# Kernel optimization log

Hardware: AMD Instinct MI355X
Metric: run time of the kernel (lower is better)

Reference implementation:

```python
import jax, jax.numpy as jnp
import numpy as np

E = 4      # num_ensemble
DIN = 256  # input_dim
D = 256    # d_model (output_dim)
B = 16
T = 1024
LN_EPS = 1e-5


def setup_inputs() -> dict:
    key = jax.random.key(0)
    ks = jax.random.split(key, 14)
    s = 0.02
    x = jax.random.normal(ks[0], (B, T, DIN), dtype=jnp.float32)
    in_proj_w = s * jax.random.normal(ks[1], (3, E, DIN, D), dtype=jnp.float32)
    in_proj_b = jnp.zeros((3, E, D), dtype=jnp.float32)
    mid_w = s * jax.random.normal(ks[2], (2, E, D, D), dtype=jnp.float32)
    mid_b = jnp.zeros((2, E, D), dtype=jnp.float32)
    ff_w1 = s * jax.random.normal(ks[3], (E, D, D), dtype=jnp.float32)
    ff_b1 = jnp.zeros((E, D), dtype=jnp.float32)
    ff_w2 = s * jax.random.normal(ks[4], (E, D, D), dtype=jnp.float32)
    ff_b2 = jnp.zeros((E, D), dtype=jnp.float32)
    ln_w = jnp.ones((E, D), dtype=jnp.float32)
    ln_b = jnp.zeros((E, D), dtype=jnp.float32)
    # LRU initializer (r_min=0.9, r_max=0.999)
    r_min, r_max = 0.9, 0.999
    u1 = jax.random.uniform(ks[5], (E, D), dtype=jnp.float32)
    u2 = jax.random.uniform(ks[6], (E, D), dtype=jnp.float32)
    nu_log = jnp.log(-0.5 * jnp.log(u1 * (r_max ** 2 - r_min ** 2) + r_min ** 2))
    theta_log = jnp.log(u2 * 2.0 * np.pi)
    # |lambda|^2 = exp(-2*exp(nu_log))
    gamma_log = jnp.log(jnp.sqrt(1.0 - jnp.exp(-2.0 * jnp.exp(nu_log))))
    params_log = jnp.stack([nu_log, theta_log, gamma_log], axis=0)  # (3,E,D)
    return {"x": x, "in_proj_w": in_proj_w, "in_proj_b": in_proj_b,
            "params_log": params_log, "mid_w": mid_w, "mid_b": mid_b,
            "ff_w1": ff_w1, "ff_b1": ff_b1, "ff_w2": ff_w2, "ff_b2": ff_b2,
            "ln_w": ln_w, "ln_b": ln_b}


def _forward(x, in_proj_w, in_proj_b, params_log, mid_w, mid_b,
             ff_w1, ff_b1, ff_w2, ff_b2, ln_w, ln_b):
    # in_proj: 3 ensemble linears -> u: (3, E, B, T, D)
    u = jnp.einsum('bti,keio->kebto', x, in_proj_w) + in_proj_b[:, :, None, None, :]
    input_real, input_imag, o = u[0], u[1], u[2]

    params = jnp.exp(params_log)           # (3,E,D)
    nu, theta, gamma = params[0], params[1], params[2]
    mag = jnp.exp(-nu)
    f_real = mag * jnp.cos(theta)          # (E,D)
    f_imag = mag * jnp.sin(theta)

    ir = gamma[:, None, None, :] * input_real  # (E,B,T,D)
    ii = gamma[:, None, None, :] * input_imag

    # complex linear recurrence h_t = f * h_{t-1} + u_t over time axis
    fr = f_real[:, None, :]                # (E,1,D) broadcast over B
    fi = f_imag[:, None, :]
    ir_t = jnp.moveaxis(ir, 2, 0)          # (T,E,B,D)
    ii_t = jnp.moveaxis(ii, 2, 0)

    def step(carry, ut):
        hr, hi = carry
        ur, ui = ut
        hr2 = fr * hr - fi * hi + ur
        hi2 = fr * hi + fi * hr + ui
        return (hr2, hi2), (hr2, hi2)

    h0 = (jnp.zeros((E, B, D), x.dtype), jnp.zeros((E, B, D), x.dtype))
    (hr_last, hi_last), (out_r_t, out_i_t) = jax.lax.scan(step, h0, (ir_t, ii_t))
    output_real = jnp.moveaxis(out_r_t, 0, 2)  # (E,B,T,D)
    output_imag = jnp.moveaxis(out_i_t, 0, 2)

    # hidden packing: (1, B, 2*E*D) with ensemble blocks concatenated, real then imag
    hr_pack = jnp.transpose(hr_last, (1, 0, 2)).reshape(B, E * D)
    hi_pack = jnp.transpose(hi_last, (1, 0, 2)).reshape(B, E * D)
    hidden = jnp.concatenate([hr_pack, hi_pack], axis=-1)[None]  # (1,B,2ED)

    # middle_proj: 2 ensemble linears applied to (real, imag)
    stacked = jnp.stack([output_real, output_imag], axis=0)  # (2,E,B,T,D)
    mid = jnp.einsum('kebtd,kedo->kebto', stacked, mid_w) + mid_b[:, :, None, None, :]
    out = mid[0] - mid[1] + o                                # (E,B,T,D)

    # EnsemblePositionWiseFeedForward (dropout=0 -> identity)
    h1 = jax.nn.gelu(jnp.einsum('ebtd,edo->ebto', out, ff_w1)
                     + ff_b1[:, None, None, :], approximate=False)
    h2 = jnp.einsum('ebtd,edo->ebto', h1, ff_w2) + ff_b2[:, None, None, :] + out
    # LayerNorm over joint (E, D) dims for each (b, t)
    mean = jnp.mean(h2, axis=(0, 3), keepdims=True)
    var = jnp.var(h2, axis=(0, 3), keepdims=True)
    out_ln = (h2 - mean) / jnp.sqrt(var + LN_EPS)
    out_ln = out_ln * ln_w[:, None, None, :] + ln_b[:, None, None, :]
    return out_ln, hidden


def reference(x, in_proj_w, in_proj_b, params_log, mid_w, mid_b,
              ff_w1, ff_b1, ff_w2, ff_b2, ln_w, ln_b):
    return _forward(x, in_proj_w, in_proj_b, params_log, mid_w, mid_b,
                    ff_w1, ff_b1, ff_w2, ff_b2, ln_w, ln_b)
```

## Files before the change

### kernel.cpp

```cpp
#include <hip/hip_runtime.h>
#include <stdint.h>

#define BT_ 16384
#define TT  1024
#define CHUNKS 32
#define CLEN   32
#define LANES  16384

typedef __bf16 bf16x8 __attribute__((ext_vector_type(8)));
typedef float  f32x4  __attribute__((ext_vector_type(4)));
typedef unsigned int u32x4 __attribute__((ext_vector_type(4)));
typedef unsigned short u16;

__device__ __forceinline__ float b2f(u16 s){
    union { float f; unsigned int u; } c; c.u = ((unsigned int)s) << 16; return c.f;
}
__device__ __forceinline__ u16 f2b(float f){
    union { float f; unsigned int u; } c; c.f = f;
    unsigned int u = c.u;
    return (u16)((u + 0x7fffu + ((u >> 16) & 1u)) >> 16);
}

__device__ __forceinline__ void gload_lds16(const u16* g, u16* lds){
    __builtin_amdgcn_global_load_lds(
        (const __attribute__((address_space(1))) void*)g,
        (__attribute__((address_space(3))) void*)lds, 16, 0, 0);
}

__global__ __launch_bounds__(256) void conv_k(const float* __restrict__ x, u16* __restrict__ xc)
{
    long i = ((long)blockIdx.x * 256 + threadIdx.x) * 8;
    float4 v0 = *reinterpret_cast<const float4*>(x + i);
    float4 v1 = *reinterpret_cast<const float4*>(x + i + 4);
    union { u16 s[8]; u32x4 v; } p;
    p.s[0] = f2b(v0.x); p.s[1] = f2b(v0.y); p.s[2] = f2b(v0.z); p.s[3] = f2b(v0.w);
    p.s[4] = f2b(v1.x); p.s[5] = f2b(v1.y); p.s[6] = f2b(v1.z); p.s[7] = f2b(v1.w);
    *reinterpret_cast<u32x4*>(xc + i) = p.v;
}

__global__ __launch_bounds__(256) void prep_w(
    const float* __restrict__ ipw, const float* __restrict__ mw,
    const float* __restrict__ fw1, const float* __restrict__ fw2,
    u16* __restrict__ d_ipw, u16* __restrict__ d_mw,
    u16* __restrict__ d_fw1, u16* __restrict__ d_fw2)
{
    __shared__ u16 tile[64][72];
    int blk = blockIdx.x;
    int w = blk >> 4, t = blk & 15;
    int tr = (t >> 2) * 64;
    int tc = (t & 3) * 64;
    const float* src; u16* dst; int ostride; float sign = 1.f;
    if (w < 12)      { src = ipw + (size_t)w * 65536; dst = d_ipw + (size_t)w * 65536; ostride = 256; }
    else if (w < 20) { int u = w - 12, c = u >> 2, e = u & 3;
                       src = mw + (size_t)u * 65536;
                       dst = d_mw + (size_t)e * 131072 + c * 256; ostride = 512;
                       if (c) sign = -1.f; }
    else if (w < 24) { int e = w - 20; src = fw1 + (size_t)e * 65536; dst = d_fw1 + (size_t)e * 65536; ostride = 256; }
    else             { int e = w - 24; src = fw2 + (size_t)e * 65536; dst = d_fw2 + (size_t)e * 65536; ostride = 256; }

    int q = threadIdx.x;
    int r = q >> 2, cb = (q & 3) * 16;
#pragma unroll
    for (int j = 0; j < 4; j++) {
        int col = cb + j * 4;
        const float4 v = *reinterpret_cast<const float4*>(src + (size_t)(tr + r) * 256 + tc + col);
        tile[r][col + 0] = f2b(v.x * sign);
        tile[r][col + 1] = f2b(v.y * sign);
        tile[r][col + 2] = f2b(v.z * sign);
        tile[r][col + 3] = f2b(v.w * sign);
    }
    __syncthreads();
    int ol = q >> 2, ib = (q & 3) * 16;
    union { u16 s[8]; u32x4 v; } p0, p1;
#pragma unroll
    for (int k = 0; k < 8; k++) { p0.s[k] = tile[ib + k][ol]; p1.s[k] = tile[ib + 8 + k][ol]; }
    u16* drow = dst + (size_t)(tc + ol) * ostride + tr + ib;
    *reinterpret_cast<u32x4*>(drow)     = p0.v;
    *reinterpret_cast<u32x4*>(drow + 8) = p1.v;
}

__global__ __launch_bounds__(256, 3) void gemm_k(
    const u16* __restrict__ A0, const u16* __restrict__ B0,
    const float* __restrict__ biasf, const u16* __restrict__ aux,
    const float* __restrict__ gamlogf, u16* __restrict__ out0,
    u16* __restrict__ out1, int K, int mode, int MT)
{
    __shared__ __align__(16) u16 Bs[64 * 256];
    __shared__ __align__(16) float fs_all[4][1024];

    int tid  = threadIdx.x;
    int wave = tid >> 6, lane = tid & 63;
    int quad = lane >> 4, l16 = lane & 15;
    int n0 = blockIdx.y * 64;
    int z = blockIdx.z;
    int e, k3 = 0;
    const u16* A;
    const u16* Bm;
    if (mode == 1) { k3 = z >> 2; e = z & 3; A = A0; }
    else           { e = z; A = A0 + (size_t)e * BT_ * K; }
    Bm = B0 + (size_t)(mode == 1 ? z : e) * 256 * K;

    int srow = lane >> 5, schunk = lane & 31;
    int nhalf = K >> 8;

    float bias_nf[4], gam_nf[4];
#pragma unroll
    for (int nf = 0; nf < 4; nf++) {
        int col = n0 + nf * 16 + l16;
        if (mode == 1) {
            bias_nf[nf] = biasf[z * 256 + col];
            gam_nf[nf] = (k3 < 2) ? expf(gamlogf[2048 + e * 256 + col]) : 1.f;
        } else if (mode == 2) {
            bias_nf[nf] = biasf[e * 256 + col] - biasf[1024 + e * 256 + col];
        } else {
            bias_nf[nf] = biasf[e * 256 + col];
        }
    }

    float* fs = fs_all[wave];
    int rr = lane >> 3, ch = lane & 7;

    for (int mt = 0; mt < MT; mt++) {
        int m0 = (blockIdx.x * MT + mt) * 128;

        f32x4 acc[2][4];
#pragma unroll
        for (int i = 0; i < 2; i++)
#pragma unroll
            for (int j = 0; j < 4; j++) acc[i][j] = (f32x4){0.f, 0.f, 0.f, 0.f};

        for (int kh = 0; kh < nhalf; kh++) {
            if (nhalf > 1 || mt == 0) {
                if (mt || kh) __syncthreads();
#pragma unroll
                for (int i = 0; i < 8; i++) {
                    int row = wave * 16 + i * 2 + srow;
                    int c = schunk ^ (row & 7);
                    gload_lds16(Bm + (size_t)(n0 + row) * K + kh * 256 + c * 8,
                                &Bs[(wave * 16 + i * 2) * 256]);
                }
                __syncthreads();
            }

            const u16* Arow0 = A + (size_t)(m0 + wave * 32 + l16) * K + kh * 256 + quad * 8;
            const u16* Arow1 = Arow0 + (size_t)16 * K;

            bf16x8 a0[8], a1[8];
#pragma unroll
            for (int p = 0; p < 4; p++) {
                union { u32x4 v; bf16x8 b; } u0, u1;
                u0.v = *reinterpret_cast<const u32x4*>(Arow0 + p * 32); a0[p] = u0.b;
                u1.v = *reinterpret_cast<const u32x4*>(Arow1 + p * 32); a1[p] = u1.b;
            }
#pragma unroll
            for (int kt = 0; kt < 8; kt++) {
                if (kt < 4) {
                    union { u32x4 v; bf16x8 b; } u0, u1;
                    u0.v = *reinterpret_cast<const u32x4*>(Arow0 + (kt + 4) * 32); a0[kt + 4] = u0.b;
                    u1.v = *reinterpret_cast<const u32x4*>(Arow1 + (kt + 4) * 32); a1[kt + 4] = u1.b;
                }
#pragma unroll
                for (int nf = 0; nf < 4; nf++) {
                    int row = nf * 16 + l16;
                    int c = (kt * 4 + quad) ^ (row & 7);
                    union { u32x4 v; bf16x8 b; } u;
                    u.v = *reinterpret_cast<const u32x4*>(&Bs[row * 256 + c * 8]);
                    acc[0][nf] = __builtin_amdgcn_mfma_f32_16x16x32_bf16(a0[kt], u.b, acc[0][nf], 0, 0, 0);
                    acc[1][nf] = __builtin_amdgcn_mfma_f32_16x16x32_bf16(a1[kt], u.b, acc[1][nf], 0, 0, 0);
                }
            }
        }

#pragma unroll
        for (int mf = 0; mf < 2; mf++) {
#pragma unroll
            for (int nf = 0; nf < 4; nf++) {
                int colsw = (nf * 16 + l16) ^ (quad * 8);
#pragma unroll
                for (int r = 0; r < 4; r++) {
                    float v = acc[mf][nf][r] + bias_nf[nf];
                    if (mode == 1) v *= gam_nf[nf];
                    if (mode == 3) v = 0.5f * v * (1.0f + erff(v * 0.70710678118654752f));
                    fs[(quad * 4 + r) * 64 + colsw] = v;
                }
            }
#pragma unroll
            for (int i = 0; i < 2; i++) {
                int rl = i * 8 + rr;
                int grow = m0 + wave * 32 + mf * 16 + rl;
                const float* sp = fs + rl * 64 + ((ch * 8) ^ ((rl >> 2) * 8));
                f32x4 v0 = *reinterpret_cast<const f32x4*>(sp);
                f32x4 v1 = *reinterpret_cast<const f32x4*>(sp + 4);
                float w[8] = { v0[0], v0[1], v0[2], v0[3], v1[0], v1[1], v1[2], v1[3] };
                u16* dstp;
                if (mode == 1) {
                    if (k3 < 2) dstp = out0 + (((size_t)(e * BT_ + grow)) * 2 + k3) * 256 + n0 + ch * 8;
                    else        dstp = out1 + ((size_t)e * BT_ + grow) * 256 + n0 + ch * 8;
                } else {
                    dstp = out0 + ((size_t)e * BT_ + grow) * 256 + n0 + ch * 8;
                }
                if (mode == 2 || mode == 4) {
                    const u16* ap = aux + ((size_t)e * BT_ + grow) * 256 + n0 + ch * 8;
                    u32x4 av = *reinterpret_cast<const u32x4*>(ap);
#pragma unroll
                    for (int j = 0; j < 4; j++) {
                        w[2 * j]     += b2f((u16)(av[j] & 0xffffu));
                        w[2 * j + 1] += b2f((u16)(av[j] >> 16));
                    }
                }
                union { u16 s[8]; u32x4 v; } p;
#pragma unroll
                for (int j = 0; j < 8; j++) p.s[j] = f2b(w[j]);
                *reinterpret_cast<u32x4*>(dstp) = p.v;
            }
        }
    }
}

__global__ __launch_bounds__(256) void scan_a(const u16* __restrict__ u,
    const float* __restrict__ plog, float2* __restrict__ carry)
{
    int l2 = blockIdx.x * 256 + threadIdx.x;
    int chunk = blockIdx.y;
    int dd = (l2 & 127) * 2, b = (l2 >> 7) & 15, e = l2 >> 11;
    float nu0 = expf(plog[e * 256 + dd]),        nu1 = expf(plog[e * 256 + dd + 1]);
    float th0 = expf(plog[1024 + e * 256 + dd]), th1 = expf(plog[1024 + e * 256 + dd + 1]);
    float m0 = expf(-nu0), m1 = expf(-nu1);
    float fr0 = m0 * cosf(th0), fi0 = m0 * sinf(th0);
    float fr1 = m1 * cosf(th1), fi1 = m1 * sinf(th1);
    size_t base = ((size_t)e * BT_ + b * TT) * 512 + (size_t)chunk * CLEN * 512 + dd;
    float hr0 = 0.f, hi0 = 0.f, hr1 = 0.f, hi1 = 0.f;
    for (int t = 0; t < CLEN; t++) {
        unsigned int wr = *reinterpret_cast<const unsigned int*>(u + base);
        unsigned int wi = *reinterpret_cast<const unsigned int*>(u + base + 256);
        float ur0 = b2f((u16)wr), ur1 = b2f((u16)(wr >> 16));
        float ui0 = b2f((u16)wi), ui1 = b2f((u16)(wi >> 16));
        float a0 = fr0 * hr0 - fi0 * hi0 + ur0;
        float b0 = fr0 * hi0 + fi0 * hr0 + ui0;
        float a1 = fr1 * hr1 - fi1 * hi1 + ur1;
        float b1 = fr1 * hi1 + fi1 * hr1 + ui1;
        hr0 = a0; hi0 = b0; hr1 = a1; hi1 = b1;
        base += 512;
    }
    size_t ci = (size_t)chunk * LANES + (size_t)e * 4096 + b * 256 + dd;
    *reinterpret_cast<float4*>(&carry[ci]) = make_float4(hr0, hi0, hr1, hi1);
}

__global__ __launch_bounds__(256) void scan_b(const float* __restrict__ plog,
                                              float2* __restrict__ carry)
{
    int l = blockIdx.x * 256 + threadIdx.x;
    int d = l & 255, e = l >> 12;
    float nu = expf(plog[e * 256 + d]);
    float th = expf(plog[1024 + e * 256 + d]);
    float magL = expf(-nu * (float)CLEN);
    float ang = th * (float)CLEN;
    float frL = magL * cosf(ang), fiL = magL * sinf(ang);
    float gr = 0.f, gi = 0.f;
    for (int j = 0; j < CHUNKS; j++) {
        float2 c = carry[(size_t)j * LANES + l];
        carry[(size_t)j * LANES + l] = make_float2(gr, gi);
        float gr2 = frL * gr - fiL * gi + c.x;
        float gi2 = frL * gi + fiL * gr + c.y;
        gr = gr2; gi = gi2;
    }
}

__global__ __launch_bounds__(256) void scan_c(u16* __restrict__ u,
    const float* __restrict__ plog, const float2* __restrict__ carry,
    float* __restrict__ outh)
{
    int l2 = blockIdx.x * 256 + threadIdx.x;
    int chunk = blockIdx.y;
    int dd = (l2 & 127) * 2, b = (l2 >> 7) & 15, e = l2 >> 11;
    float nu0 = expf(plog[e * 256 + dd]),        nu1 = expf(plog[e * 256 + dd + 1]);
    float th0 = expf(plog[1024 + e * 256 + dd]), th1 = expf(plog[1024 + e * 256 + dd + 1]);
    float m0 = expf(-nu0), m1 = expf(-nu1);
    float fr0 = m0 * cosf(th0), fi0 = m0 * sinf(th0);
    float fr1 = m1 * cosf(th1), fi1 = m1 * sinf(th1);
    size_t base = ((size_t)e * BT_ + b * TT) * 512 + (size_t)chunk * CLEN * 512 + dd;
    size_t ci = (size_t)chunk * LANES + (size_t)e * 4096 + b * 256 + dd;
    float4 c0 = *reinterpret_cast<const float4*>(&carry[ci]);
    float hr0 = c0.x, hi0 = c0.y, hr1 = c0.z, hi1 = c0.w;
    for (int t = 0; t < CLEN; t++) {
        unsigned int wr = *reinterpret_cast<const unsigned int*>(u + base);
        unsigned int wi = *reinterpret_cast<const unsigned int*>(u + base + 256);
        float ur0 = b2f((u16)wr), ur1 = b2f((u16)(wr >> 16));
        float ui0 = b2f((u16)wi), ui1 = b2f((u16)(wi >> 16));
        float a0 = fr0 * hr0 - fi0 * hi0 + ur0;
        float b0 = fr0 * hi0 + fi0 * hr0 + ui0;
        float a1 = fr1 * hr1 - fi1 * hi1 + ur1;
        float b1 = fr1 * hi1 + fi1 * hr1 + ui1;
        hr0 = a0; hi0 = b0; hr1 = a1; hi1 = b1;
        *reinterpret_cast<unsigned int*>(u + base) =
            (unsigned int)f2b(hr0) | ((unsigned int)f2b(hr1) << 16);
        *reinterpret_cast<unsigned int*>(u + base + 256) =
            (unsigned int)f2b(hi0) | ((unsigned int)f2b(hi1) << 16);
        base += 512;
    }
    if (chunk == CHUNKS - 1) {
        float* oh = outh + (size_t)4 * BT_ * 256;
        *reinterpret_cast<float2*>(&oh[b * 2048 + e * 256 + dd])        = make_float2(hr0, hr1);
        *reinterpret_cast<float2*>(&oh[b * 2048 + 1024 + e * 256 + dd]) = make_float2(hi0, hi1);
    }
}

__global__ __launch_bounds__(256) void ln_k(const u16* __restrict__ h2,
    const float* __restrict__ lnw, const float* __restrict__ lnb,
    float* __restrict__ out)
{
    int r = blockIdx.x;
    int d = threadIdx.x;
    float v[4]; float s1 = 0.f, s2 = 0.f;
#pragma unroll
    for (int e = 0; e < 4; e++) {
        float x = b2f(h2[((size_t)e * BT_ + r) * 256 + d]);
        v[e] = x; s1 += x; s2 += x * x;
    }
#pragma unroll
    for (int off = 32; off; off >>= 1) {
        s1 += __shfl_down(s1, off, 64);
        s2 += __shfl_down(s2, off, 64);
    }
    __shared__ float sm[8];
    int wave = threadIdx.x >> 6, lane = threadIdx.x & 63;
    if (lane == 0) { sm[wave] = s1; sm[4 + wave] = s2; }
    __syncthreads();
    float S1 = sm[0] + sm[1] + sm[2] + sm[3];
    float S2 = sm[4] + sm[5] + sm[6] + sm[7];
    float mean = S1 * (1.0f / 1024.0f);
    float var = S2 * (1.0f / 1024.0f) - mean * mean;
    float rstd = rsqrtf(var + 1e-5f);
#pragma unroll
    for (int e = 0; e < 4; e++) {
        float o = (v[e] - mean) * rstd * lnw[e * 256 + d] + lnb[e * 256 + d];
        out[((size_t)e * BT_ + r) * 256 + d] = o;
    }
}

extern "C" void kernel_launch(void* const* d_in, const int* in_sizes, int n_in,
                              void* d_out, int out_size, void* d_ws, size_t ws_size,
                              hipStream_t stream)
{
    const float* x    = (const float*)d_in[0];
    const float* ipw  = (const float*)d_in[1];
    const float* ipb  = (const float*)d_in[2];
    const float* plog = (const float*)d_in[3];
    const float* mw   = (const float*)d_in[4];
    const float* mb   = (const float*)d_in[5];
    const float* fw1  = (const float*)d_in[6];
    const float* fb1  = (const float*)d_in[7];
    const float* fw2  = (const float*)d_in[8];
    const float* fb2  = (const float*)d_in[9];
    const float* lnw  = (const float*)d_in[10];
    const float* lnb  = (const float*)d_in[11];
    float* out = (float*)d_out;

    u16* W = (u16*)d_ws;
    u16* buf_u    = W;
    u16* buf_out  = W + (size_t)33554432;
    u16* xc       = W + (size_t)33554432;
    float2* carry = (float2*)(W + (size_t)37748736);
    u16* buf_mw_t = W + (size_t)50331648;
    u16* c_ipw_t  = W + (size_t)50855936;
    u16* c_fw1_t  = W + (size_t)51642368;
    u16* c_fw2_t  = W + (size_t)51904512;
    u16* scratch  = (u16*)d_out;

    conv_k<<<2048, 256, 0, stream>>>(x, xc);
    prep_w<<<448, 256, 0, stream>>>(ipw, mw, fw1, fw2, c_ipw_t, buf_mw_t, c_fw1_t, c_fw2_t);
    gemm_k<<<dim3(32, 4, 12), 256, 0, stream>>>(xc, c_ipw_t, ipb, nullptr, plog, buf_u, scratch, 256, 1, 4);
    scan_a<<<dim3(32, CHUNKS), 256, 0, stream>>>(buf_u, plog, carry);
    scan_b<<<64, 256, 0, stream>>>(plog, carry);
    scan_c<<<dim3(32, CHUNKS), 256, 0, stream>>>(buf_u, plog, carry, out);
    gemm_k<<<dim3(64, 4, 4), 256, 0, stream>>>(buf_u, buf_mw_t, mb, scratch, nullptr, buf_out, nullptr, 512, 2, 2);
    gemm_k<<<dim3(64, 4, 4), 256, 0, stream>>>(buf_out, c_fw1_t, fb1, nullptr, nullptr, scratch, nullptr, 256, 3, 2);
    gemm_k<<<dim3(64, 4, 4), 256, 0, stream>>>(scratch, c_fw2_t, fb2, buf_out, nullptr, buf_u, nullptr, 256, 4, 2);
    ln_k<<<16384, 256, 0, stream>>>(buf_u, lnw, lnb, out);
}
```

Before: 329.8 us.

## Double GEMM M-tile per wave to 64 rows with rolling A-fragment prefetch

Each wave now computes 64 rows (four 16-row MFMA fragments) instead of 32, so every B fragment read from LDS feeds four MFMAs rather than two, and the grid x-dimension is halved to match. The A-operand register buffer changes from a full 8-step preload to a one-step-ahead rolling prefetch, which holds register pressure down despite the doubled accumulators. The trade-off is fewer blocks per launch, less latency hiding from the shallower A prefetch, and possibly lower occupancy from the larger accumulator set.

```diff
diff --git a/kernel.cpp b/kernel.cpp
--- a/kernel.cpp
+++ b/kernel.cpp
@@ -121,11 +121,11 @@
     int rr = lane >> 3, ch = lane & 7;
 
     for (int mt = 0; mt < MT; mt++) {
-        int m0 = (blockIdx.x * MT + mt) * 128;
-
-        f32x4 acc[2][4];
-#pragma unroll
-        for (int i = 0; i < 2; i++)
+        int m0 = (blockIdx.x * MT + mt) * 256;
+
+        f32x4 acc[4][4];
+#pragma unroll
+        for (int i = 0; i < 4; i++)
 #pragma unroll
             for (int j = 0; j < 4; j++) acc[i][j] = (f32x4){0.f, 0.f, 0.f, 0.f};
 
@@ -142,22 +142,25 @@
                 __syncthreads();
             }
 
-            const u16* Arow0 = A + (size_t)(m0 + wave * 32 + l16) * K + kh * 256 + quad * 8;
-            const u16* Arow1 = Arow0 + (size_t)16 * K;
-
-            bf16x8 a0[8], a1[8];
-#pragma unroll
-            for (int p = 0; p < 4; p++) {
-                union { u32x4 v; bf16x8 b; } u0, u1;
-                u0.v = *reinterpret_cast<const u32x4*>(Arow0 + p * 32); a0[p] = u0.b;
-                u1.v = *reinterpret_cast<const u32x4*>(Arow1 + p * 32); a1[p] = u1.b;
-            }
+            const u16* Ar0 = A + (size_t)(m0 + wave * 64 + l16) * K + kh * 256 + quad * 8;
+            const u16* Ar1 = Ar0 + (size_t)16 * K;
+            const u16* Ar2 = Ar0 + (size_t)32 * K;
+            const u16* Ar3 = Ar0 + (size_t)48 * K;
+
+            bf16x8 ac0, ac1, ac2, ac3, an0, an1, an2, an3;
+            { union { u32x4 v; bf16x8 b; } u;
+              u.v = *reinterpret_cast<const u32x4*>(Ar0); ac0 = u.b;
+              u.v = *reinterpret_cast<const u32x4*>(Ar1); ac1 = u.b;
+              u.v = *reinterpret_cast<const u32x4*>(Ar2); ac2 = u.b;
+              u.v = *reinterpret_cast<const u32x4*>(Ar3); ac3 = u.b; }
 #pragma unroll
             for (int kt = 0; kt < 8; kt++) {
-                if (kt < 4) {
-                    union { u32x4 v; bf16x8 b; } u0, u1;
-                    u0.v = *reinterpret_cast<const u32x4*>(Arow0 + (kt + 4) * 32); a0[kt + 4] = u0.b;
-                    u1.v = *reinterpret_cast<const u32x4*>(Arow1 + (kt + 4) * 32); a1[kt + 4] = u1.b;
+                if (kt < 7) {
+                    union { u32x4 v; bf16x8 b; } u;
+                    u.v = *reinterpret_cast<const u32x4*>(Ar0 + (kt + 1) * 32); an0 = u.b;
+                    u.v = *reinterpret_cast<const u32x4*>(Ar1 + (kt + 1) * 32); an1 = u.b;
+                    u.v = *reinterpret_cast<const u32x4*>(Ar2 + (kt + 1) * 32); an2 = u.b;
+                    u.v = *reinterpret_cast<const u32x4*>(Ar3 + (kt + 1) * 32); an3 = u.b;
                 }
 #pragma unroll
                 for (int nf = 0; nf < 4; nf++) {
@@ -165,20 +168,23 @@
                     int c = (kt * 4 + quad) ^ (row & 7);
                     union { u32x4 v; bf16x8 b; } u;
                     u.v = *reinterpret_cast<const u32x4*>(&Bs[row * 256 + c * 8]);
-                    acc[0][nf] = __builtin_amdgcn_mfma_f32_16x16x32_bf16(a0[kt], u.b, acc[0][nf], 0, 0, 0);
-                    acc[1][nf] = __builtin_amdgcn_mfma_f32_16x16x32_bf16(a1[kt], u.b, acc[1][nf], 0, 0, 0);
-                }
+                    acc[0][nf] = __builtin_amdgcn_mfma_f32_16x16x32_bf16(ac0, u.b, acc[0][nf], 0, 0, 0);
+                    acc[1][nf] = __builtin_amdgcn_mfma_f32_16x16x32_bf16(ac1, u.b, acc[1][nf], 0, 0, 0);
+                    acc[2][nf] = __builtin_amdgcn_mfma_f32_16x16x32_bf16(ac2, u.b, acc[2][nf], 0, 0, 0);
+                    acc[3][nf] = __builtin_amdgcn_mfma_f32_16x16x32_bf16(ac3, u.b, acc[3][nf], 0, 0, 0);
+                }
+                ac0 = an0; ac1 = an1; ac2 = an2; ac3 = an3;
             }
         }
 
 #pragma unroll
-        for (int mf = 0; mf < 2; mf++) {
+        for (int s = 0; s < 4; s++) {
 #pragma unroll
             for (int nf = 0; nf < 4; nf++) {
                 int colsw = (nf * 16 + l16) ^ (quad * 8);
 #pragma unroll
                 for (int r = 0; r < 4; r++) {
-                    float v = acc[mf][nf][r] + bias_nf[nf];
+                    float v = acc[s][nf][r] + bias_nf[nf];
                     if (mode == 1) v *= gam_nf[nf];
                     if (mode == 3) v = 0.5f * v * (1.0f + erff(v * 0.70710678118654752f));
                     fs[(quad * 4 + r) * 64 + colsw] = v;
@@ -187,7 +193,7 @@
 #pragma unroll
             for (int i = 0; i < 2; i++) {
                 int rl = i * 8 + rr;
-                int grow = m0 + wave * 32 + mf * 16 + rl;
+                int grow = m0 + wave * 64 + s * 16 + rl;
                 const float* sp = fs + rl * 64 + ((ch * 8) ^ ((rl >> 2) * 8));
                 f32x4 v0 = *reinterpret_cast<const f32x4*>(sp);
                 f32x4 v1 = *reinterpret_cast<const f32x4*>(sp + 4);
@@ -369,12 +375,12 @@
 
     conv_k<<<2048, 256, 0, stream>>>(x, xc);
     prep_w<<<448, 256, 0, stream>>>(ipw, mw, fw1, fw2, c_ipw_t, buf_mw_t, c_fw1_t, c_fw2_t);
-    gemm_k<<<dim3(32, 4, 12), 256, 0, stream>>>(xc, c_ipw_t, ipb, nullptr, plog, buf_u, scratch, 256, 1, 4);
+    gemm_k<<<dim3(16, 4, 12), 256, 0, stream>>>(xc, c_ipw_t, ipb, nullptr, plog, buf_u, scratch, 256, 1, 4);
     scan_a<<<dim3(32, CHUNKS), 256, 0, stream>>>(buf_u, plog, carry);
     scan_b<<<64, 256, 0, stream>>>(plog, carry);
     scan_c<<<dim3(32, CHUNKS), 256, 0, stream>>>(buf_u, plog, carry, out);
-    gemm_k<<<dim3(64, 4, 4), 256, 0, stream>>>(buf_u, buf_mw_t, mb, scratch, nullptr, buf_out, nullptr, 512, 2, 2);
-    gemm_k<<<dim3(64, 4, 4), 256, 0, stream>>>(buf_out, c_fw1_t, fb1, nullptr, nullptr, scratch, nullptr, 256, 3, 2);
-    gemm_k<<<dim3(64, 4, 4), 256, 0, stream>>>(scratch, c_fw2_t, fb2, buf_out, nullptr, buf_u, nullptr, 256, 4, 2);
+    gemm_k<<<dim3(32, 4, 4), 256, 0, stream>>>(buf_u, buf_mw_t, mb, scratch, nullptr, buf_out, nullptr, 512, 2, 2);
+    gemm_k<<<dim3(32, 4, 4), 256, 0, stream>>>(buf_out, c_fw1_t, fb1, nullptr, nullptr, scratch, nullptr, 256, 3, 2);
+    gemm_k<<<dim3(32, 4, 4), 256, 0, stream>>>(scratch, c_fw2_t, fb2, buf_out, nullptr, buf_u, nullptr, 256, 4, 2);
     ln_k<<<16384, 256, 0, stream>>>(buf_u, lnw, lnb, out);
 }
```

After: 319.5 us. 3.1% less time.
